# Performance work log

Hardware: AMD Instinct MI355X
Metric: run time of the kernel (lower is better)

## Reference

```python
import jax, jax.numpy as jnp
import numpy as np

E = 1024
H = 16
D = E // H  # head_dim = 64
B, L, S = 2, 2048, 2048


def setup_inputs() -> dict:
    key = jax.random.key(0)
    ks = jax.random.split(key, 10)
    scale = 1.0 / np.sqrt(E)
    return {
        "x": jax.random.normal(ks[0], (B, L, E), jnp.float32),
        "context": jax.random.normal(ks[1], (B, S, E), jnp.float32),
        "Wq": jax.random.normal(ks[2], (E, E), jnp.float32) * scale,
        "bq": jnp.zeros((E,), jnp.float32),
        "Wk": jax.random.normal(ks[3], (E, E), jnp.float32) * scale,
        "bk": jnp.zeros((E,), jnp.float32),
        "Wv": jax.random.normal(ks[4], (E, E), jnp.float32) * scale,
        "bv": jnp.zeros((E,), jnp.float32),
        "Wp": jax.random.normal(ks[5], (E, E), jnp.float32) * scale,
        "bp": jnp.zeros((E,), jnp.float32),
    }


def reference(x, context, Wq, bq, Wk, bk, Wv, bv, Wp, bp):
    b, l, _ = x.shape
    s = context.shape[1]
    # linear projections then split heads: [B, H, L/S, D]
    q = (x @ Wq + bq).reshape(b, l, H, D).transpose(0, 2, 1, 3)
    k = (context @ Wk + bk).reshape(b, s, H, D).transpose(0, 2, 1, 3)
    v = (context @ Wv + bv).reshape(b, s, H, D).transpose(0, 2, 1, 3)
    # scores [B, H, L, S]
    attn = jnp.einsum("bhld,bhsd->bhls", q, k) / jnp.sqrt(jnp.float32(D))
    attn = jax.nn.softmax(attn, axis=-1)
    # dropout is identity in eval mode
    out = jnp.einsum("bhls,bhsd->bhld", attn, v)
    out = out.transpose(0, 2, 1, 3).reshape(b, l, E)
    return out @ Wp + bp
```

## Files before the change

kernel.cpp:

```cpp
#include <hip/hip_runtime.h>
#include <math.h>

#define B_ 2
#define L_ 2048
#define S_ 2048
#define E_ 1024
#define H_ 16
#define D_ 64
#define SC_ 0.180336880111120f

typedef unsigned short u16;
typedef unsigned int u32;
typedef __attribute__((ext_vector_type(8))) short short8;
typedef __attribute__((ext_vector_type(4))) float floatx4;

__device__ __forceinline__ u16 f2bf(float f) {
    union { float f; unsigned u; } a; a.f = f;
    unsigned r = a.u + 0x7FFFu + ((a.u >> 16) & 1u);
    return (u16)(r >> 16);
}

__device__ __forceinline__ u32 cvt_pk_bf16(float lo, float hi) {
    u32 d;
    asm("v_cvt_pk_bf16_f32 %0, %1, %2" : "=v"(d) : "v"(lo), "v"(hi));
    return d;
}

__device__ __forceinline__ void pl32swap(u32& a, u32& b) {
    asm("v_permlane32_swap_b32 %0, %1" : "+v"(a), "+v"(b));
}
__device__ __forceinline__ void pl16swap(u32& a, u32& b) {
    asm("v_permlane16_swap_b32 %0, %1" : "+v"(a), "+v"(b));
}

__device__ __forceinline__ void glds16(const u16* g, u16* l) {
    __builtin_amdgcn_global_load_lds(
        (const __attribute__((address_space(1))) void*)g,
        (__attribute__((address_space(3))) void*)l, 16, 0, 0);
}

__global__ void cast_bf16_kernel(const float* __restrict__ x, const float* __restrict__ ctx,
                                 u16* __restrict__ Xb, u16* __restrict__ Cb) {
    const float* src = blockIdx.y ? ctx : x;
    u16* dst = blockIdx.y ? Cb : Xb;
    int i = blockIdx.x * 256 + threadIdx.x;
    float4 u0 = ((const float4*)src)[2 * i];
    float4 u1 = ((const float4*)src)[2 * i + 1];
    uint4 o;
    o.x = cvt_pk_bf16(u0.x, u0.y);
    o.y = cvt_pk_bf16(u0.z, u0.w);
    o.z = cvt_pk_bf16(u1.x, u1.y);
    o.w = cvt_pk_bf16(u1.z, u1.w);
    ((uint4*)dst)[i] = o;
}

__global__ void transpose_cast_kernel(const float* __restrict__ Wq, const float* __restrict__ Wk,
                                      const float* __restrict__ Wv, const float* __restrict__ Wp,
                                      u16* __restrict__ WqT, u16* __restrict__ WkT,
                                      u16* __restrict__ WvT, u16* __restrict__ WpT) {
    const int z = blockIdx.z;
    const float* W = z == 0 ? Wq : (z == 1 ? Wk : (z == 2 ? Wv : Wp));
    u16* Wt = z == 0 ? WqT : (z == 1 ? WkT : (z == 2 ? WvT : WpT));
    __shared__ float tile[32][33];
    const int bx = blockIdx.x * 32, by = blockIdx.y * 32;
    const int tx = threadIdx.x, ty = threadIdx.y;
#pragma unroll
    for (int j = 0; j < 4; ++j)
        tile[ty + j * 8][tx] = W[(size_t)(by + ty + j * 8) * E_ + bx + tx];
    __syncthreads();
#pragma unroll
    for (int j = 0; j < 4; ++j)
        Wt[(size_t)(bx + ty + j * 8) * E_ + by + tx] = f2bf(tile[tx][ty + j * 8]);
}

__device__ __forceinline__ void xcd_remap(int bx, int by, int& m_idx, int& n_idx) {
    int lin = bx + 8 * by;
    int c8 = lin & 7;
    int g = lin >> 3;
    m_idx = c8 + 8 * (g & 3);
    n_idx = g >> 2;
}

__global__ __launch_bounds__(256, 2) void qkv_gemm_kernel(
    const u16* __restrict__ Xb, const u16* __restrict__ Cb,
    const u16* __restrict__ WqT, const u16* __restrict__ WkT, const u16* __restrict__ WvT,
    const float* __restrict__ bq, const float* __restrict__ bk, const float* __restrict__ bv,
    u16* __restrict__ Qb, u16* __restrict__ Kb, u16* __restrict__ Vtb) {
    __shared__ __align__(16) u16 As[2][128 * 64];
    __shared__ __align__(16) u16 Bs[2][128 * 64];

    const int z = blockIdx.z;
    const u16* A  = z == 0 ? Xb : Cb;
    const u16* Bt = z == 0 ? WqT : (z == 1 ? WkT : WvT);
    const float* bias = z == 0 ? bq : (z == 1 ? bk : bv);
    const float scale = z == 0 ? SC_ : 1.0f;

    const int tid = threadIdx.x;
    const int lane = tid & 63;
    const int wv = tid >> 6;
    const int wm = wv >> 1, wn = wv & 1;
    const int qd = lane >> 4, lr = lane & 15;
    int m_idx, n_idx;
    xcd_remap(blockIdx.x, blockIdx.y, m_idx, n_idx);
    const int m0 = m_idx * 128, n0 = n_idx * 128;
    const int lrow = lane >> 3;
    const int gu = (lane & 7) ^ lrow;

    floatx4 acc[4][4];
#pragma unroll
    for (int i = 0; i < 4; ++i)
#pragma unroll
        for (int j = 0; j < 4; ++j) {
            floatx4 zz = {0.f, 0.f, 0.f, 0.f};
            acc[i][j] = zz;
        }

#define STAGE_AB(buf, kb)                                                          \
    {                                                                              \
        _Pragma("unroll") for (int j = 0; j < 4; ++j) {                            \
            int c = wv * 4 + j;                                                    \
            glds16(A + (size_t)(m0 + c * 8 + lrow) * E_ + (kb) + gu * 8,           \
                   &As[buf][c * 512]);                                             \
            glds16(Bt + (size_t)(n0 + c * 8 + lrow) * E_ + (kb) + gu * 8,          \
                   &Bs[buf][c * 512]);                                             \
        }                                                                          \
    }

    STAGE_AB(0, 0)
    __syncthreads();

    for (int t = 0; t < 16; ++t) {
        const int cur = t & 1;
        if (t + 1 < 16) STAGE_AB(cur ^ 1, (t + 1) * 64)

        short8 af[4][2], bf[4][2];
#pragma unroll
        for (int mi = 0; mi < 4; ++mi)
#pragma unroll
            for (int kk = 0; kk < 2; ++kk) {
                int row = wm * 64 + mi * 16 + lr;
                int u = (kk * 4 + qd) ^ (lr & 7);
                af[mi][kk] = *(const short8*)(&As[cur][row * 64 + u * 8]);
            }
#pragma unroll
        for (int ni = 0; ni < 4; ++ni)
#pragma unroll
            for (int kk = 0; kk < 2; ++kk) {
                int row = wn * 64 + ni * 16 + lr;
                int u = (kk * 4 + qd) ^ (lr & 7);
                bf[ni][kk] = *(const short8*)(&Bs[cur][row * 64 + u * 8]);
            }
        __builtin_amdgcn_s_setprio(1);
#pragma unroll
        for (int kk = 0; kk < 2; ++kk)
#pragma unroll
            for (int mi = 0; mi < 4; ++mi)
#pragma unroll
                for (int ni = 0; ni < 4; ++ni)
                    acc[mi][ni] = __builtin_amdgcn_mfma_f32_16x16x32_bf16(
                        af[mi][kk], bf[ni][kk], acc[mi][ni], 0, 0, 0);
        __builtin_amdgcn_s_setprio(0);

        __syncthreads();
    }

    u16* Cq = z == 0 ? Qb : Kb;
#pragma unroll
    for (int mi = 0; mi < 4; ++mi) {
#pragma unroll
        for (int ni = 0; ni < 4; ++ni) {
            int col = n0 + wn * 64 + ni * 16 + lr;
            float bv_ = bias[col];
            if (z == 2) {
                int row0 = m0 + wm * 64 + mi * 16 + qd * 4;
                int bidx = row0 >> 11;
                int sloc = row0 & (S_ - 1);
                u16 h0 = f2bf(acc[mi][ni][0] + bv_);
                u16 h1 = f2bf(acc[mi][ni][1] + bv_);
                u16 h2 = f2bf(acc[mi][ni][2] + bv_);
                u16 h3 = f2bf(acc[mi][ni][3] + bv_);
                uint2 pk;
                pk.x = h0 | ((unsigned)h1 << 16);
                pk.y = h2 | ((unsigned)h3 << 16);
                *(uint2*)&Vtb[((size_t)(bidx * E_ + col)) * S_ + sloc] = pk;
            } else {
#pragma unroll
                for (int r = 0; r < 4; ++r) {
                    int row = m0 + wm * 64 + mi * 16 + qd * 4 + r;
                    Cq[(size_t)row * E_ + col] = f2bf((acc[mi][ni][r] + bv_) * scale);
                }
            }
        }
    }
#undef STAGE_AB
}

__global__ __launch_bounds__(256, 4) void flash_attn_kernel(
    const u16* __restrict__ Q, const u16* __restrict__ Kg,
    const u16* __restrict__ Vtg, u16* __restrict__ Opart, float* __restrict__ lpart) {
    __shared__ __align__(16) u16 Ks[2][64 * 64];
    __shared__ __align__(16) u16 Vs[2][64 * 64];

    const int tid = threadIdx.x;
    const int lane = tid & 63;
    const int wv = tid >> 6;
    const int qd = lane >> 4, lr = lane & 15;

    const int lin = blockIdx.x + 16 * (blockIdx.y + 32 * blockIdx.z);
    const int c8 = lin & 7;
    const int slot = lin >> 3;
    const int qx = slot & 15;
    const int grp = c8 + 8 * (slot >> 4);
    const int bh = grp & 31;
    const int z = grp >> 5;
    const int b = bh >> 4, h = bh & 15;
    const int q0 = qx * 128;
    const int sbeg = z * (S_ / 2);

    u16* Op = Opart + (size_t)z * (B_ * L_ * E_);
    float* lp = lpart + (size_t)z * (B_ * H_ * L_);

    const u16* Kbase = Kg + (size_t)(b * S_) * E_ + h * D_;
    const u16* Vbase = Vtg + (size_t)(b * E_ + h * D_) * S_;

    const int lrow = lane >> 3;
    const int gu = (lane & 7) ^ lrow;

#pragma unroll
    for (int j = 0; j < 2; ++j) {
        int c = wv * 2 + j;
        glds16(Kbase + (size_t)(sbeg + c * 8 + lrow) * E_ + gu * 8, &Ks[0][c * 512]);
        glds16(Vbase + (size_t)(c * 8 + lrow) * S_ + sbeg + gu * 8, &Vs[0][c * 512]);
    }

    short8 qf[2][2];
#pragma unroll
    for (int mi = 0; mi < 2; ++mi)
#pragma unroll
        for (int kk = 0; kk < 2; ++kk)
            qf[mi][kk] = *(const short8*)(Q + (size_t)(b * L_ + q0 + wv * 32 + mi * 16 + lr) * E_ +
                                          h * D_ + kk * 32 + qd * 8);

    floatx4 o_acc[2][4];
    float l_acc[2] = {0.f, 0.f};
#pragma unroll
    for (int mi = 0; mi < 2; ++mi)
#pragma unroll
        for (int nt = 0; nt < 4; ++nt) {
            floatx4 z4 = {0.f, 0.f, 0.f, 0.f};
            o_acc[mi][nt] = z4;
        }

    __syncthreads();

    const int NIT = (S_ / 2) / 64;

    for (int it = 0; it < NIT; ++it) {
        const int cur = it & 1;
        if (it + 1 < NIT) {
            int s1 = sbeg + (it + 1) * 64;
#pragma unroll
            for (int j = 0; j < 2; ++j) {
                int c = wv * 2 + j;
                glds16(Kbase + (size_t)(s1 + c * 8 + lrow) * E_ + gu * 8, &Ks[cur ^ 1][c * 512]);
                glds16(Vbase + (size_t)(c * 8 + lrow) * S_ + s1 + gu * 8, &Vs[cur ^ 1][c * 512]);
            }
        }

        floatx4 s_[2][4];
        __builtin_amdgcn_s_setprio(1);
#pragma unroll
        for (int nt = 0; nt < 4; ++nt) {
            int krow = nt * 16 + lr;
            short8 kb0 = *(const short8*)(&Ks[cur][krow * 64 + ((qd) ^ (lr & 7)) * 8]);
            short8 kb1 = *(const short8*)(&Ks[cur][krow * 64 + ((4 + qd) ^ (lr & 7)) * 8]);
#pragma unroll
            for (int mi = 0; mi < 2; ++mi) {
                floatx4 zz = {0.f, 0.f, 0.f, 0.f};
                zz = __builtin_amdgcn_mfma_f32_16x16x32_bf16(kb0, qf[mi][0], zz, 0, 0, 0);
                zz = __builtin_amdgcn_mfma_f32_16x16x32_bf16(kb1, qf[mi][1], zz, 0, 0, 0);
                s_[mi][nt] = zz;
            }
        }
        __builtin_amdgcn_s_setprio(0);

        short8 pf[2][2];
#pragma unroll
        for (int mi = 0; mi < 2; ++mi) {
            u32 dg[4][2];
            float ls = 0.f;
#pragma unroll
            for (int nt = 0; nt < 4; ++nt) {
                float p0 = __builtin_amdgcn_exp2f(s_[mi][nt][0]);
                float p1 = __builtin_amdgcn_exp2f(s_[mi][nt][1]);
                float p2 = __builtin_amdgcn_exp2f(s_[mi][nt][2]);
                float p3 = __builtin_amdgcn_exp2f(s_[mi][nt][3]);
                ls += (p0 + p1) + (p2 + p3);
                dg[nt][0] = cvt_pk_bf16(p0, p1);
                dg[nt][1] = cvt_pk_bf16(p2, p3);
            }
            l_acc[mi] += ls;
#pragma unroll
            for (int kk = 0; kk < 2; ++kk) {
                u32 x0 = dg[2 * kk][0], y0 = dg[2 * kk + 1][0];
                pl32swap(x0, y0);
                pl16swap(x0, y0);
                u32 x1 = dg[2 * kk][1], y1 = dg[2 * kk + 1][1];
                pl32swap(x1, y1);
                pl16swap(x1, y1);
                union { u32 d[4]; short8 v; } u;
                u.d[0] = x0; u.d[1] = x1; u.d[2] = y0; u.d[3] = y1;
                pf[mi][kk] = u.v;
            }
        }

        __builtin_amdgcn_s_setprio(1);
#pragma unroll
        for (int nt = 0; nt < 4; ++nt) {
            int vrow = nt * 16 + lr;
            short8 vb0 = *(const short8*)(&Vs[cur][vrow * 64 + ((qd) ^ (lr & 7)) * 8]);
            short8 vb1 = *(const short8*)(&Vs[cur][vrow * 64 + ((4 + qd) ^ (lr & 7)) * 8]);
#pragma unroll
            for (int mi = 0; mi < 2; ++mi) {
                o_acc[mi][nt] = __builtin_amdgcn_mfma_f32_16x16x32_bf16(pf[mi][0], vb0, o_acc[mi][nt], 0, 0, 0);
                o_acc[mi][nt] = __builtin_amdgcn_mfma_f32_16x16x32_bf16(pf[mi][1], vb1, o_acc[mi][nt], 0, 0, 0);
            }
        }
        __builtin_amdgcn_s_setprio(0);

        __syncthreads();
    }

    float linv[2][4];
#pragma unroll
    for (int mi = 0; mi < 2; ++mi) {
        float l = l_acc[mi];
        l += __shfl_xor(l, 16);
        l += __shfl_xor(l, 32);
        if (lane < 16)
            lp[(size_t)(b * H_ + h) * L_ + q0 + wv * 32 + mi * 16 + lane] = l;
        float il = 1.0f / l;
#pragma unroll
        for (int r = 0; r < 4; ++r) linv[mi][r] = __shfl(il, qd * 4 + r);
    }

#pragma unroll
    for (int mi = 0; mi < 2; ++mi)
#pragma unroll
        for (int nt = 0; nt < 4; ++nt)
#pragma unroll
            for (int r = 0; r < 4; ++r) {
                int row = q0 + wv * 32 + mi * 16 + qd * 4 + r;
                int col = h * D_ + nt * 16 + lr;
                Op[(size_t)(b * L_ + row) * E_ + col] = f2bf(o_acc[mi][nt][r] * linv[mi][r]);
            }
}

__global__ __launch_bounds__(256, 2) void out_gemm_kernel(
    const u16* __restrict__ O1, const u16* __restrict__ O2,
    const float* __restrict__ l1, const float* __restrict__ l2,
    const u16* __restrict__ WpT, const float* __restrict__ bp,
    float* __restrict__ out) {
    __shared__ __align__(16) u16 As[2][128 * 64];
    __shared__ __align__(16) u16 Bs[2][128 * 64];

    const int tid = threadIdx.x;
    const int lane = tid & 63;
    const int wv = tid >> 6;
    const int wm = wv >> 1, wn = wv & 1;
    const int qd = lane >> 4, lr = lane & 15;
    int m_idx, n_idx;
    xcd_remap(blockIdx.x, blockIdx.y, m_idx, n_idx);
    const int m0 = m_idx * 128, n0 = n_idx * 128;
    const int lrow = lane >> 3;
    const int gu = (lane & 7) ^ lrow;

    floatx4 acc[4][4];
#pragma unroll
    for (int i = 0; i < 4; ++i)
#pragma unroll
        for (int j = 0; j < 4; ++j) {
            floatx4 zz = {0.f, 0.f, 0.f, 0.f};
            acc[i][j] = zz;
        }

    uint4 p1[4], p2[4];
    float la_[4], lb_[4];

#define LOAD_AO(tt)                                                                \
    {                                                                              \
        _Pragma("unroll") for (int j = 0; j < 4; ++j) {                            \
            int c = wv * 4 + j;                                                    \
            int row = m0 + c * 8 + lrow;                                           \
            int col = (tt)*64 + gu * 8;                                            \
            p1[j] = *(const uint4*)(O1 + (size_t)row * E_ + col);                  \
            p2[j] = *(const uint4*)(O2 + (size_t)row * E_ + col);                  \
            int li = (row >> 11) * (H_ * L_) + (tt)*L_ + (row & (L_ - 1));         \
            la_[j] = l1[li];                                                       \
            lb_[j] = l2[li];                                                       \
        }                                                                          \
    }

#define WRITE_AO(buf)                                                              \
    {                                                                              \
        _Pragma("unroll") for (int j = 0; j < 4; ++j) {                            \
            int c = wv * 4 + j;                                                    \
            float s = 1.0f / (la_[j] + lb_[j]);                                    \
            float w1 = la_[j] * s, w2 = lb_[j] * s;                                \
            const u32* pa = (const u32*)&p1[j];                                    \
            const u32* pb = (const u32*)&p2[j];                                    \
            uint4 o;                                                               \
            u32* po = (u32*)&o;                                                    \
            _Pragma("unroll") for (int d = 0; d < 4; ++d) {                        \
                union { u32 u; float f; } x0, x1, y0, y1;                          \
                x0.u = pa[d] << 16; x1.u = pa[d] & 0xFFFF0000u;                    \
                y0.u = pb[d] << 16; y1.u = pb[d] & 0xFFFF0000u;                    \
                po[d] = cvt_pk_bf16(x0.f * w1 + y0.f * w2, x1.f * w1 + y1.f * w2); \
            }                                                                      \
            *(uint4*)(&As[buf][c * 512 + lane * 8]) = o;                           \
        }                                                                          \
    }

#define STAGE_BO(buf, kb)                                                          \
    {                                                                              \
        _Pragma("unroll") for (int j = 0; j < 4; ++j) {                            \
            int c = wv * 4 + j;                                                    \
            glds16(WpT + (size_t)(n0 + c * 8 + lrow) * E_ + (kb) + gu * 8,         \
                   &Bs[buf][c * 512]);                                             \
        }                                                                          \
    }

    LOAD_AO(0)
    STAGE_BO(0, 0)
    WRITE_AO(0)
    __syncthreads();

    for (int t = 0; t < 16; ++t) {
        const int cur = t & 1;
        if (t + 1 < 16) {
            STAGE_BO(cur ^ 1, (t + 1) * 64)
            LOAD_AO(t + 1)
        }

        short8 af[4][2], bf[4][2];
#pragma unroll
        for (int mi = 0; mi < 4; ++mi)
#pragma unroll
            for (int kk = 0; kk < 2; ++kk) {
                int row = wm * 64 + mi * 16 + lr;
                int u = (kk * 4 + qd) ^ (lr & 7);
                af[mi][kk] = *(const short8*)(&As[cur][row * 64 + u * 8]);
            }
#pragma unroll
        for (int ni = 0; ni < 4; ++ni)
#pragma unroll
            for (int kk = 0; kk < 2; ++kk) {
                int row = wn * 64 + ni * 16 + lr;
                int u = (kk * 4 + qd) ^ (lr & 7);
                bf[ni][kk] = *(const short8*)(&Bs[cur][row * 64 + u * 8]);
            }
        __builtin_amdgcn_s_setprio(1);
#pragma unroll
        for (int kk = 0; kk < 2; ++kk)
#pragma unroll
            for (int mi = 0; mi < 4; ++mi)
#pragma unroll
                for (int ni = 0; ni < 4; ++ni)
                    acc[mi][ni] = __builtin_amdgcn_mfma_f32_16x16x32_bf16(
                        af[mi][kk], bf[ni][kk], acc[mi][ni], 0, 0, 0);
        __builtin_amdgcn_s_setprio(0);

        if (t + 1 < 16) WRITE_AO(cur ^ 1)
        __syncthreads();
    }

#pragma unroll
    for (int mi = 0; mi < 4; ++mi)
#pragma unroll
        for (int ni = 0; ni < 4; ++ni) {
            int col = n0 + wn * 64 + ni * 16 + lr;
            float bv_ = bp[col];
#pragma unroll
            for (int r = 0; r < 4; ++r) {
                int row = m0 + wm * 64 + mi * 16 + qd * 4 + r;
                out[(size_t)row * E_ + col] = acc[mi][ni][r] + bv_;
            }
        }
#undef LOAD_AO
#undef WRITE_AO
#undef STAGE_BO
}

extern "C" void kernel_launch(void* const* d_in, const int* in_sizes, int n_in,
                              void* d_out, int out_size, void* d_ws, size_t ws_size,
                              hipStream_t stream) {
    const float* x   = (const float*)d_in[0];
    const float* ctx = (const float*)d_in[1];
    const float* Wq  = (const float*)d_in[2];
    const float* bq  = (const float*)d_in[3];
    const float* Wk  = (const float*)d_in[4];
    const float* bk  = (const float*)d_in[5];
    const float* Wv  = (const float*)d_in[6];
    const float* bv  = (const float*)d_in[7];
    const float* Wp  = (const float*)d_in[8];
    const float* bp  = (const float*)d_in[9];
    float* out = (float*)d_out;

    u16* WqT = (u16*)d_ws;
    u16* WkT = WqT + 1048576;
    u16* WvT = WkT + 1048576;
    u16* WpT = WvT + 1048576;
    u16* Qb  = WpT + 1048576;
    u16* Kb  = Qb + 4194304;
    u16* Vtb = Kb + 4194304;
    u16* Xb  = Vtb + 4194304;
    u16* Cb  = Xb + 4194304;
    u16* Opart = Xb;
    float* lpart = (float*)(Cb + 4194304);
    (void)ws_size; (void)in_sizes; (void)n_in; (void)out_size;

    cast_bf16_kernel<<<dim3(2048, 2), 256, 0, stream>>>(x, ctx, Xb, Cb);
    transpose_cast_kernel<<<dim3(32, 32, 4), dim3(32, 8), 0, stream>>>(
        Wq, Wk, Wv, Wp, WqT, WkT, WvT, WpT);

    qkv_gemm_kernel<<<dim3(8, 32, 3), 256, 0, stream>>>(
        Xb, Cb, WqT, WkT, WvT, bq, bk, bv, Qb, Kb, Vtb);

    flash_attn_kernel<<<dim3(L_ / 128, B_ * H_, 2), 256, 0, stream>>>(
        Qb, Kb, Vtb, Opart, lpart);

    out_gemm_kernel<<<dim3(8, 32), 256, 0, stream>>>(
        Opart, Opart + 4194304, lpart, lpart + B_ * H_ * L_, WpT, bp, out);
}
```

Before: 216.3 us.

## Merge prep kernels, compute softmax row sums via MFMA, shrink out-GEMM M tile

Folds the activation cast and the weight transpose-cast into one launch, which removes a kernel launch boundary. In flash attention the scalar per-row exp sum and cross-lane shuffles are replaced by an extra MFMA of P against a ones vector, so the row sums come out already in accumulator layout. The output GEMM moves from 128x128 to 64x128 tiles with twice as many blocks, to fill more CUs. These changes add MFMA work per iteration and lower data reuse in the output GEMM.

```diff
diff --git a/kernel.cpp b/kernel.cpp
--- a/kernel.cpp
+++ b/kernel.cpp
@@ -39,38 +39,44 @@
         (__attribute__((address_space(3))) void*)l, 16, 0, 0);
 }
 
-__global__ void cast_bf16_kernel(const float* __restrict__ x, const float* __restrict__ ctx,
-                                 u16* __restrict__ Xb, u16* __restrict__ Cb) {
-    const float* src = blockIdx.y ? ctx : x;
-    u16* dst = blockIdx.y ? Cb : Xb;
-    int i = blockIdx.x * 256 + threadIdx.x;
-    float4 u0 = ((const float4*)src)[2 * i];
-    float4 u1 = ((const float4*)src)[2 * i + 1];
-    uint4 o;
-    o.x = cvt_pk_bf16(u0.x, u0.y);
-    o.y = cvt_pk_bf16(u0.z, u0.w);
-    o.z = cvt_pk_bf16(u1.x, u1.y);
-    o.w = cvt_pk_bf16(u1.z, u1.w);
-    ((uint4*)dst)[i] = o;
-}
-
-__global__ void transpose_cast_kernel(const float* __restrict__ Wq, const float* __restrict__ Wk,
-                                      const float* __restrict__ Wv, const float* __restrict__ Wp,
-                                      u16* __restrict__ WqT, u16* __restrict__ WkT,
-                                      u16* __restrict__ WvT, u16* __restrict__ WpT) {
-    const int z = blockIdx.z;
-    const float* W = z == 0 ? Wq : (z == 1 ? Wk : (z == 2 ? Wv : Wp));
-    u16* Wt = z == 0 ? WqT : (z == 1 ? WkT : (z == 2 ? WvT : WpT));
+__global__ void prep_kernel(const float* __restrict__ x, const float* __restrict__ ctx,
+                            u16* __restrict__ Xb, u16* __restrict__ Cb,
+                            const float* __restrict__ Wq, const float* __restrict__ Wk,
+                            const float* __restrict__ Wv, const float* __restrict__ Wp,
+                            u16* __restrict__ WqT, u16* __restrict__ WkT,
+                            u16* __restrict__ WvT, u16* __restrict__ WpT) {
     __shared__ float tile[32][33];
-    const int bx = blockIdx.x * 32, by = blockIdx.y * 32;
-    const int tx = threadIdx.x, ty = threadIdx.y;
-#pragma unroll
-    for (int j = 0; j < 4; ++j)
-        tile[ty + j * 8][tx] = W[(size_t)(by + ty + j * 8) * E_ + bx + tx];
-    __syncthreads();
-#pragma unroll
-    for (int j = 0; j < 4; ++j)
-        Wt[(size_t)(bx + ty + j * 8) * E_ + by + tx] = f2bf(tile[tx][ty + j * 8]);
+    const int bid = blockIdx.x;
+    const int tid = threadIdx.x;
+    if (bid < 4096) {
+        const int sub = bid;
+        const float* src = sub < 2048 ? x : ctx;
+        u16* dst = sub < 2048 ? Xb : Cb;
+        int i = (sub & 2047) * 256 + tid;
+        float4 u0 = ((const float4*)src)[2 * i];
+        float4 u1 = ((const float4*)src)[2 * i + 1];
+        uint4 o;
+        o.x = cvt_pk_bf16(u0.x, u0.y);
+        o.y = cvt_pk_bf16(u0.z, u0.w);
+        o.z = cvt_pk_bf16(u1.x, u1.y);
+        o.w = cvt_pk_bf16(u1.z, u1.w);
+        ((uint4*)dst)[i] = o;
+    } else {
+        const int t = bid - 4096;
+        const int z = t >> 10;
+        const int rem = t & 1023;
+        const float* W = z == 0 ? Wq : (z == 1 ? Wk : (z == 2 ? Wv : Wp));
+        u16* Wt = z == 0 ? WqT : (z == 1 ? WkT : (z == 2 ? WvT : WpT));
+        const int bx = (rem & 31) * 32, by = (rem >> 5) * 32;
+        const int tx = tid & 31, ty = tid >> 5;
+#pragma unroll
+        for (int j = 0; j < 4; ++j)
+            tile[ty + j * 8][tx] = W[(size_t)(by + ty + j * 8) * E_ + bx + tx];
+        __syncthreads();
+#pragma unroll
+        for (int j = 0; j < 4; ++j)
+            Wt[(size_t)(bx + ty + j * 8) * E_ + by + tx] = f2bf(tile[tx][ty + j * 8]);
+    }
 }
 
 __device__ __forceinline__ void xcd_remap(int bx, int by, int& m_idx, int& n_idx) {
@@ -241,15 +247,21 @@
             qf[mi][kk] = *(const short8*)(Q + (size_t)(b * L_ + q0 + wv * 32 + mi * 16 + lr) * E_ +
                                           h * D_ + kk * 32 + qd * 8);
 
+    const short one_bf = (short)0x3F80;
+    short8 ones8 = {one_bf, one_bf, one_bf, one_bf, one_bf, one_bf, one_bf, one_bf};
+
     floatx4 o_acc[2][4];
-    float l_acc[2] = {0.f, 0.f};
-#pragma unroll
-    for (int mi = 0; mi < 2; ++mi)
+    floatx4 l4[2];
+#pragma unroll
+    for (int mi = 0; mi < 2; ++mi) {
 #pragma unroll
         for (int nt = 0; nt < 4; ++nt) {
             floatx4 z4 = {0.f, 0.f, 0.f, 0.f};
             o_acc[mi][nt] = z4;
         }
+        floatx4 z4 = {0.f, 0.f, 0.f, 0.f};
+        l4[mi] = z4;
+    }
 
     __syncthreads();
 
@@ -288,18 +300,15 @@
 #pragma unroll
         for (int mi = 0; mi < 2; ++mi) {
             u32 dg[4][2];
-            float ls = 0.f;
 #pragma unroll
             for (int nt = 0; nt < 4; ++nt) {
                 float p0 = __builtin_amdgcn_exp2f(s_[mi][nt][0]);
                 float p1 = __builtin_amdgcn_exp2f(s_[mi][nt][1]);
                 float p2 = __builtin_amdgcn_exp2f(s_[mi][nt][2]);
                 float p3 = __builtin_amdgcn_exp2f(s_[mi][nt][3]);
-                ls += (p0 + p1) + (p2 + p3);
                 dg[nt][0] = cvt_pk_bf16(p0, p1);
                 dg[nt][1] = cvt_pk_bf16(p2, p3);
             }
-            l_acc[mi] += ls;
 #pragma unroll
             for (int kk = 0; kk < 2; ++kk) {
                 u32 x0 = dg[2 * kk][0], y0 = dg[2 * kk + 1][0];
@@ -316,6 +325,11 @@
 
         __builtin_amdgcn_s_setprio(1);
 #pragma unroll
+        for (int mi = 0; mi < 2; ++mi) {
+            l4[mi] = __builtin_amdgcn_mfma_f32_16x16x32_bf16(pf[mi][0], ones8, l4[mi], 0, 0, 0);
+            l4[mi] = __builtin_amdgcn_mfma_f32_16x16x32_bf16(pf[mi][1], ones8, l4[mi], 0, 0, 0);
+        }
+#pragma unroll
         for (int nt = 0; nt < 4; ++nt) {
             int vrow = nt * 16 + lr;
             short8 vb0 = *(const short8*)(&Vs[cur][vrow * 64 + ((qd) ^ (lr & 7)) * 8]);
@@ -334,14 +348,13 @@
     float linv[2][4];
 #pragma unroll
     for (int mi = 0; mi < 2; ++mi) {
-        float l = l_acc[mi];
-        l += __shfl_xor(l, 16);
-        l += __shfl_xor(l, 32);
-        if (lane < 16)
-            lp[(size_t)(b * H_ + h) * L_ + q0 + wv * 32 + mi * 16 + lane] = l;
-        float il = 1.0f / l;
-#pragma unroll
-        for (int r = 0; r < 4; ++r) linv[mi][r] = __shfl(il, qd * 4 + r);
+        if (lr == 0) {
+#pragma unroll
+            for (int r = 0; r < 4; ++r)
+                lp[(size_t)(b * H_ + h) * L_ + q0 + wv * 32 + mi * 16 + qd * 4 + r] = l4[mi][r];
+        }
+#pragma unroll
+        for (int r = 0; r < 4; ++r) linv[mi][r] = 1.0f / l4[mi][r];
     }
 
 #pragma unroll
@@ -361,7 +374,7 @@
     const float* __restrict__ l1, const float* __restrict__ l2,
     const u16* __restrict__ WpT, const float* __restrict__ bp,
     float* __restrict__ out) {
-    __shared__ __align__(16) u16 As[2][128 * 64];
+    __shared__ __align__(16) u16 As[2][64 * 64];
     __shared__ __align__(16) u16 Bs[2][128 * 64];
 
     const int tid = threadIdx.x;
@@ -369,28 +382,32 @@
     const int wv = tid >> 6;
     const int wm = wv >> 1, wn = wv & 1;
     const int qd = lane >> 4, lr = lane & 15;
-    int m_idx, n_idx;
-    xcd_remap(blockIdx.x, blockIdx.y, m_idx, n_idx);
-    const int m0 = m_idx * 128, n0 = n_idx * 128;
+
+    int lin = blockIdx.x + 8 * blockIdx.y;
+    int c8 = lin & 7;
+    int g = lin >> 3;
+    const int m_idx = c8 + 8 * (g & 7);
+    const int n_idx = g >> 3;
+    const int m0 = m_idx * 64, n0 = n_idx * 128;
     const int lrow = lane >> 3;
     const int gu = (lane & 7) ^ lrow;
 
-    floatx4 acc[4][4];
-#pragma unroll
-    for (int i = 0; i < 4; ++i)
+    floatx4 acc[2][4];
+#pragma unroll
+    for (int i = 0; i < 2; ++i)
 #pragma unroll
         for (int j = 0; j < 4; ++j) {
             floatx4 zz = {0.f, 0.f, 0.f, 0.f};
             acc[i][j] = zz;
         }
 
-    uint4 p1[4], p2[4];
-    float la_[4], lb_[4];
+    uint4 p1[2], p2[2];
+    float la_[2], lb_[2];
 
 #define LOAD_AO(tt)                                                                \
     {                                                                              \
-        _Pragma("unroll") for (int j = 0; j < 4; ++j) {                            \
-            int c = wv * 4 + j;                                                    \
+        _Pragma("unroll") for (int j = 0; j < 2; ++j) {                            \
+            int c = wv * 2 + j;                                                    \
             int row = m0 + c * 8 + lrow;                                           \
             int col = (tt)*64 + gu * 8;                                            \
             p1[j] = *(const uint4*)(O1 + (size_t)row * E_ + col);                  \
@@ -403,8 +420,8 @@
 
 #define WRITE_AO(buf)                                                              \
     {                                                                              \
-        _Pragma("unroll") for (int j = 0; j < 4; ++j) {                            \
-            int c = wv * 4 + j;                                                    \
+        _Pragma("unroll") for (int j = 0; j < 2; ++j) {                            \
+            int c = wv * 2 + j;                                                    \
             float s = 1.0f / (la_[j] + lb_[j]);                                    \
             float w1 = la_[j] * s, w2 = lb_[j] * s;                                \
             const u32* pa = (const u32*)&p1[j];                                    \
@@ -442,12 +459,12 @@
             LOAD_AO(t + 1)
         }
 
-        short8 af[4][2], bf[4][2];
-#pragma unroll
-        for (int mi = 0; mi < 4; ++mi)
+        short8 af[2][2], bf[4][2];
+#pragma unroll
+        for (int mi = 0; mi < 2; ++mi)
 #pragma unroll
             for (int kk = 0; kk < 2; ++kk) {
-                int row = wm * 64 + mi * 16 + lr;
+                int row = wm * 32 + mi * 16 + lr;
                 int u = (kk * 4 + qd) ^ (lr & 7);
                 af[mi][kk] = *(const short8*)(&As[cur][row * 64 + u * 8]);
             }
@@ -463,7 +480,7 @@
 #pragma unroll
         for (int kk = 0; kk < 2; ++kk)
 #pragma unroll
-            for (int mi = 0; mi < 4; ++mi)
+            for (int mi = 0; mi < 2; ++mi)
 #pragma unroll
                 for (int ni = 0; ni < 4; ++ni)
                     acc[mi][ni] = __builtin_amdgcn_mfma_f32_16x16x32_bf16(
@@ -475,14 +492,14 @@
     }
 
 #pragma unroll
-    for (int mi = 0; mi < 4; ++mi)
+    for (int mi = 0; mi < 2; ++mi)
 #pragma unroll
         for (int ni = 0; ni < 4; ++ni) {
             int col = n0 + wn * 64 + ni * 16 + lr;
             float bv_ = bp[col];
 #pragma unroll
             for (int r = 0; r < 4; ++r) {
-                int row = m0 + wm * 64 + mi * 16 + qd * 4 + r;
+                int row = m0 + wm * 32 + mi * 16 + qd * 4 + r;
                 out[(size_t)row * E_ + col] = acc[mi][ni][r] + bv_;
             }
         }
@@ -519,9 +536,8 @@
     float* lpart = (float*)(Cb + 4194304);
     (void)ws_size; (void)in_sizes; (void)n_in; (void)out_size;
 
-    cast_bf16_kernel<<<dim3(2048, 2), 256, 0, stream>>>(x, ctx, Xb, Cb);
-    transpose_cast_kernel<<<dim3(32, 32, 4), dim3(32, 8), 0, stream>>>(
-        Wq, Wk, Wv, Wp, WqT, WkT, WvT, WpT);
+    prep_kernel<<<dim3(8192), 256, 0, stream>>>(
+        x, ctx, Xb, Cb, Wq, Wk, Wv, Wp, WqT, WkT, WvT, WpT);
 
     qkv_gemm_kernel<<<dim3(8, 32, 3), 256, 0, stream>>>(
         Xb, Cb, WqT, WkT, WvT, bq, bk, bv, Qb, Kb, Vtb);
@@ -529,6 +545,6 @@
     flash_attn_kernel<<<dim3(L_ / 128, B_ * H_, 2), 256, 0, stream>>>(
         Qb, Kb, Vtb, Opart, lpart);
 
-    out_gemm_kernel<<<dim3(8, 32), 256, 0, stream>>>(
+    out_gemm_kernel<<<dim3(8, 64), 256, 0, stream>>>(
         Opart, Opart + 4194304, lpart, lpart + B_ * H_ * L_, WpT, bp, out);
 }
```

Measured after the change: 205.7 us. 1.05x faster.
